# Performance work log

Hardware: AMD Instinct MI355X
Metric: run time of the kernel (lower is better)

The kernel has to match this reference:

```python
import jax, jax.numpy as jnp
import numpy as np

N_NODES = 100000
N_EDGES = 1600000
D_FEAT = 32


def setup_inputs() -> dict:
    key = jax.random.key(0)
    k1, k2 = jax.random.split(key)
    x = jax.random.normal(k1, (N_NODES, D_FEAT), dtype=jnp.float32)
    edge_index = jax.random.randint(k2, (2, N_EDGES), 0, N_NODES, dtype=jnp.int64)
    return {"x": x, "edge_index": edge_index}


def reference(x, edge_index):
    # SparseTensor(row=edge_index[0], col=edge_index[1]).matmul(x, reduce='mean')
    # out[i] = mean_{e: row[e]==i} x[col[e]], 0 for isolated rows.
    row, col = edge_index[0], edge_index[1]
    msg_sum = jax.ops.segment_sum(x[col], row, num_segments=N_NODES)  # [N, D]
    deg = jax.ops.segment_sum(jnp.ones((row.shape[0],), dtype=x.dtype), row,
                              num_segments=N_NODES)  # [N]
    denom = jnp.maximum(deg, jnp.asarray(1, dtype=x.dtype))
    return msg_sum / denom[:, None]
```

## Files before the change

kernel.cpp:

```cpp
#include <hip/hip_runtime.h>
#include <hip/hip_fp16.h>

#define D_FEAT 32
#define BNODES 64
#define LOG_BN 6
#define CHUNK 16384
#define BIG 1024
#define ECHUNK 2048
#define CAP 2048
#define CMASK 0x1FFFFu

__global__ void prep_kernel(const float* __restrict__ x, __half* __restrict__ xh,
                            int* __restrict__ cnt, int n8, int nb) {
    int i = blockIdx.x * blockDim.x + threadIdx.x;
    if (i < nb) cnt[i] = 0;
    if (i < n8) {
        float4 v = ((const float4*)x)[i];
        __half2 h0 = __floats2half2_rn(v.x, v.y);
        __half2 h1 = __floats2half2_rn(v.z, v.w);
        uint2 u;
        u.x = *reinterpret_cast<unsigned*>(&h0);
        u.y = *reinterpret_cast<unsigned*>(&h1);
        ((uint2*)xh)[i] = u;
    }
}

__global__ void __launch_bounds__(BIG) build_kernel(const int* __restrict__ row,
                                                    const int* __restrict__ col,
                                                    int* __restrict__ cnt,
                                                    unsigned* __restrict__ packed,
                                                    int E, int nb) {
    extern __shared__ int shmem[];
    int* hist = shmem;
    int* base = shmem + nb;
    int t = threadIdx.x;
    int blk = blockIdx.x;
    for (int i = t; i < nb; i += BIG) hist[i] = 0;

    int s = blk * CHUNK;
    int e_end = min(E, s + CHUNK);

    int4 r[4], c[4];
    if (s + CHUNK <= E) {
        #pragma unroll
        for (int k = 0; k < 4; ++k) {
            int e = s + t * 4 + k * (BIG * 4);
            r[k] = *(const int4*)&row[e];
            c[k] = *(const int4*)&col[e];
        }
    } else {
        #pragma unroll
        for (int k = 0; k < 4; ++k) {
            int e = s + t * 4 + k * (BIG * 4);
            r[k].x = (e + 0 < e_end) ? row[e + 0] : -1;
            r[k].y = (e + 1 < e_end) ? row[e + 1] : -1;
            r[k].z = (e + 2 < e_end) ? row[e + 2] : -1;
            r[k].w = (e + 3 < e_end) ? row[e + 3] : -1;
            c[k].x = (e + 0 < e_end) ? col[e + 0] : 0;
            c[k].y = (e + 1 < e_end) ? col[e + 1] : 0;
            c[k].z = (e + 2 < e_end) ? col[e + 2] : 0;
            c[k].w = (e + 3 < e_end) ? col[e + 3] : 0;
        }
    }
    __syncthreads();

    #pragma unroll
    for (int k = 0; k < 4; ++k) {
        if (r[k].x >= 0) atomicAdd(&hist[r[k].x >> LOG_BN], 1);
        if (r[k].y >= 0) atomicAdd(&hist[r[k].y >> LOG_BN], 1);
        if (r[k].z >= 0) atomicAdd(&hist[r[k].z >> LOG_BN], 1);
        if (r[k].w >= 0) atomicAdd(&hist[r[k].w >> LOG_BN], 1);
    }
    __syncthreads();

    for (int i = t; i < nb; i += BIG) {
        int h = hist[i];
        base[i] = h ? (i * CAP + atomicAdd(&cnt[i], h)) : 0;
    }
    __syncthreads();

    #define EMIT(rr, cc)                                                      \
        if ((rr) >= 0) {                                                      \
            int b_ = (rr) >> LOG_BN;                                          \
            int slot_ = base[b_] + atomicAdd(&hist[b_], -1) - 1;              \
            packed[slot_] = ((unsigned)((rr) & (BNODES - 1)) << 17) |         \
                            (unsigned)(cc);                                   \
        }
    #pragma unroll
    for (int k = 0; k < 4; ++k) {
        EMIT(r[k].x, c[k].x); EMIT(r[k].y, c[k].y);
        EMIT(r[k].z, c[k].z); EMIT(r[k].w, c[k].w);
    }
    #undef EMIT
}

__global__ void __launch_bounds__(512) phase2_kernel(const __half* __restrict__ xh,
                                                     const unsigned* __restrict__ packed,
                                                     const int* __restrict__ cnt,
                                                     float* __restrict__ out, int N) {
    __shared__ unsigned scol[ECHUNK];
    __shared__ int hist[BNODES];
    __shared__ int hoff[BNODES];
    int t = threadIdx.x;
    int b = blockIdx.x;
    int s = b * CAP;
    int n = cnt[b];
    int node = t >> 3;
    int j = t & 7;
    const uint2* xh2 = (const uint2*)xh;

    float4 acc = make_float4(0.f, 0.f, 0.f, 0.f);
    int mydeg = 0;

    for (int cs = 0; cs < n; cs += ECHUNK) {
        int m = min(ECHUNK, n - cs);
        if (t < BNODES) hist[t] = 0;
        __syncthreads();
        for (int i = t; i < m; i += 512)
            atomicAdd(&hist[packed[s + cs + i] >> 17], 1);
        __syncthreads();
        if (t < 64) {
            int v = hist[t];
            int sum = v;
            #pragma unroll
            for (int off = 1; off < 64; off <<= 1) {
                int w = __shfl_up(sum, off);
                if (t >= off) sum += w;
            }
            hoff[t] = sum - v;
        }
        __syncthreads();
        int mcount = hist[node];
        int mbase = hoff[node];
        mydeg += mcount;
        __syncthreads();
        for (int i = t; i < m; i += 512) {
            unsigned p = packed[s + cs + i];
            int r = p >> 17;
            int slot = hoff[r] + atomicAdd(&hist[r], -1) - 1;
            scol[slot] = p;
        }
        __syncthreads();

        #define ACCUM(u)                                                       \
            {                                                                  \
                __half2 ha = *reinterpret_cast<const __half2*>(&(u).x);        \
                __half2 hb = *reinterpret_cast<const __half2*>(&(u).y);        \
                float2 fa = __half22float2(ha);                                \
                float2 fb = __half22float2(hb);                                \
                acc.x += fa.x; acc.y += fa.y; acc.z += fb.x; acc.w += fb.y;    \
            }

        int i = 0;
        for (; i + 7 < mcount; i += 8) {
            unsigned cc0 = scol[mbase + i + 0] & CMASK;
            unsigned cc1 = scol[mbase + i + 1] & CMASK;
            unsigned cc2 = scol[mbase + i + 2] & CMASK;
            unsigned cc3 = scol[mbase + i + 3] & CMASK;
            unsigned cc4 = scol[mbase + i + 4] & CMASK;
            unsigned cc5 = scol[mbase + i + 5] & CMASK;
            unsigned cc6 = scol[mbase + i + 6] & CMASK;
            unsigned cc7 = scol[mbase + i + 7] & CMASK;
            uint2 u0 = xh2[cc0 * 8 + j];
            uint2 u1 = xh2[cc1 * 8 + j];
            uint2 u2 = xh2[cc2 * 8 + j];
            uint2 u3 = xh2[cc3 * 8 + j];
            uint2 u4 = xh2[cc4 * 8 + j];
            uint2 u5 = xh2[cc5 * 8 + j];
            uint2 u6 = xh2[cc6 * 8 + j];
            uint2 u7 = xh2[cc7 * 8 + j];
            ACCUM(u0); ACCUM(u1); ACCUM(u2); ACCUM(u3);
            ACCUM(u4); ACCUM(u5); ACCUM(u6); ACCUM(u7);
        }
        for (; i < mcount; ++i) {
            unsigned cc = scol[mbase + i] & CMASK;
            uint2 u = xh2[cc * 8 + j];
            ACCUM(u);
        }
        #undef ACCUM
        __syncthreads();
    }

    int gnode = b * BNODES + node;
    if (gnode < N) {
        float invd = 1.0f / fmaxf((float)mydeg, 1.0f);
        float4 v;
        v.x = acc.x * invd; v.y = acc.y * invd;
        v.z = acc.z * invd; v.w = acc.w * invd;
        ((float4*)out)[(size_t)gnode * 8 + j] = v;
    }
}


extern "C" void kernel_launch(void* const* d_in, const int* in_sizes, int n_in,
                              void* d_out, int out_size, void* d_ws, size_t ws_size,
                              hipStream_t stream) {
    const float* x = (const float*)d_in[0];
    const int* edge_index = (const int*)d_in[1];

    int E = in_sizes[1] / 2;
    const int* row = edge_index;
    const int* col = edge_index + E;
    int N = in_sizes[0] / D_FEAT;

    float* out = (float*)d_out;

    int nb = (N + BNODES - 1) / BNODES;
    int nchunks = (E + CHUNK - 1) / CHUNK;
    int n8 = in_sizes[0] / 4;

    int* cnt = (int*)d_ws;
    __half* xh = (__half*)(cnt + ((nb + 1023) & ~1023));
    unsigned* packed = (unsigned*)((char*)xh + (size_t)in_sizes[0] * sizeof(__half));

    int prep_grid = (max(n8, nb) + 255) / 256;
    prep_kernel<<<prep_grid, 256, 0, stream>>>(x, xh, cnt, n8, nb);

    size_t lds = (size_t)2 * nb * sizeof(int);
    build_kernel<<<nchunks, BIG, lds, stream>>>(row, col, cnt, packed, E, nb);
    phase2_kernel<<<nb, 512, 0, stream>>>(xh, packed, cnt, out, N);
}
```

Baseline: 56.23 us.

## Fuse fp16 conversion into build kernel and single-pass phase2 with register-held edges

```diff
diff --git a/kernel.cpp b/kernel.cpp
--- a/kernel.cpp
+++ b/kernel.cpp
@@ -6,30 +6,22 @@
 #define LOG_BN 6
 #define CHUNK 16384
 #define BIG 1024
-#define ECHUNK 2048
-#define CAP 2048
+#define CAP 1536
+#define ECHUNK CAP
 #define CMASK 0x1FFFFu
 
-__global__ void prep_kernel(const float* __restrict__ x, __half* __restrict__ xh,
-                            int* __restrict__ cnt, int n8, int nb) {
+__global__ void zero_kernel(int* __restrict__ p, int n) {
     int i = blockIdx.x * blockDim.x + threadIdx.x;
-    if (i < nb) cnt[i] = 0;
-    if (i < n8) {
-        float4 v = ((const float4*)x)[i];
-        __half2 h0 = __floats2half2_rn(v.x, v.y);
-        __half2 h1 = __floats2half2_rn(v.z, v.w);
-        uint2 u;
-        u.x = *reinterpret_cast<unsigned*>(&h0);
-        u.y = *reinterpret_cast<unsigned*>(&h1);
-        ((uint2*)xh)[i] = u;
-    }
+    if (i < n) p[i] = 0;
 }
 
 __global__ void __launch_bounds__(BIG) build_kernel(const int* __restrict__ row,
                                                     const int* __restrict__ col,
+                                                    const float* __restrict__ x,
+                                                    __half* __restrict__ xh,
                                                     int* __restrict__ cnt,
                                                     unsigned* __restrict__ packed,
-                                                    int E, int nb) {
+                                                    int E, int nb, int n8) {
     extern __shared__ int shmem[];
     int* hist = shmem;
     int* base = shmem + nb;
@@ -92,6 +84,17 @@
         EMIT(r[k].z, c[k].z); EMIT(r[k].w, c[k].w);
     }
     #undef EMIT
+
+    int gstride = gridDim.x * BIG;
+    for (int i = blk * BIG + t; i < n8; i += gstride) {
+        float4 v = ((const float4*)x)[i];
+        __half2 h0 = __floats2half2_rn(v.x, v.y);
+        __half2 h1 = __floats2half2_rn(v.z, v.w);
+        uint2 u;
+        u.x = *reinterpret_cast<unsigned*>(&h0);
+        u.y = *reinterpret_cast<unsigned*>(&h1);
+        ((uint2*)xh)[i] = u;
+    }
 }
 
 __global__ void __launch_bounds__(512) phase2_kernel(const __half* __restrict__ xh,
@@ -109,81 +112,88 @@
     int j = t & 7;
     const uint2* xh2 = (const uint2*)xh;
 
-    float4 acc = make_float4(0.f, 0.f, 0.f, 0.f);
-    int mydeg = 0;
-
-    for (int cs = 0; cs < n; cs += ECHUNK) {
-        int m = min(ECHUNK, n - cs);
-        if (t < BNODES) hist[t] = 0;
-        __syncthreads();
-        for (int i = t; i < m; i += 512)
-            atomicAdd(&hist[packed[s + cs + i] >> 17], 1);
-        __syncthreads();
-        if (t < 64) {
-            int v = hist[t];
-            int sum = v;
-            #pragma unroll
-            for (int off = 1; off < 64; off <<= 1) {
-                int w = __shfl_up(sum, off);
-                if (t >= off) sum += w;
-            }
-            hoff[t] = sum - v;
-        }
-        __syncthreads();
-        int mcount = hist[node];
-        int mbase = hoff[node];
-        mydeg += mcount;
-        __syncthreads();
-        for (int i = t; i < m; i += 512) {
-            unsigned p = packed[s + cs + i];
+    if (t < BNODES) hist[t] = 0;
+    __syncthreads();
+
+    unsigned pv[3];
+    int nv = 0;
+    #pragma unroll
+    for (int k = 0; k < 3; ++k) {
+        int i = t + k * 512;
+        if (i < n) {
+            unsigned p = packed[s + i];
+            pv[nv++] = p;
+            atomicAdd(&hist[p >> 17], 1);
+        }
+    }
+    __syncthreads();
+
+    if (t < 64) {
+        int v = hist[t];
+        int sum = v;
+        #pragma unroll
+        for (int off = 1; off < 64; off <<= 1) {
+            int w = __shfl_up(sum, off);
+            if (t >= off) sum += w;
+        }
+        hoff[t] = sum - v;
+    }
+    __syncthreads();
+    int mcount = hist[node];
+    int mbase = hoff[node];
+    __syncthreads();
+
+    #pragma unroll
+    for (int k = 0; k < 3; ++k) {
+        if (k < nv) {
+            unsigned p = pv[k];
             int r = p >> 17;
             int slot = hoff[r] + atomicAdd(&hist[r], -1) - 1;
             scol[slot] = p;
         }
-        __syncthreads();
-
-        #define ACCUM(u)                                                       \
-            {                                                                  \
-                __half2 ha = *reinterpret_cast<const __half2*>(&(u).x);        \
-                __half2 hb = *reinterpret_cast<const __half2*>(&(u).y);        \
-                float2 fa = __half22float2(ha);                                \
-                float2 fb = __half22float2(hb);                                \
-                acc.x += fa.x; acc.y += fa.y; acc.z += fb.x; acc.w += fb.y;    \
-            }
-
-        int i = 0;
-        for (; i + 7 < mcount; i += 8) {
-            unsigned cc0 = scol[mbase + i + 0] & CMASK;
-            unsigned cc1 = scol[mbase + i + 1] & CMASK;
-            unsigned cc2 = scol[mbase + i + 2] & CMASK;
-            unsigned cc3 = scol[mbase + i + 3] & CMASK;
-            unsigned cc4 = scol[mbase + i + 4] & CMASK;
-            unsigned cc5 = scol[mbase + i + 5] & CMASK;
-            unsigned cc6 = scol[mbase + i + 6] & CMASK;
-            unsigned cc7 = scol[mbase + i + 7] & CMASK;
-            uint2 u0 = xh2[cc0 * 8 + j];
-            uint2 u1 = xh2[cc1 * 8 + j];
-            uint2 u2 = xh2[cc2 * 8 + j];
-            uint2 u3 = xh2[cc3 * 8 + j];
-            uint2 u4 = xh2[cc4 * 8 + j];
-            uint2 u5 = xh2[cc5 * 8 + j];
-            uint2 u6 = xh2[cc6 * 8 + j];
-            uint2 u7 = xh2[cc7 * 8 + j];
-            ACCUM(u0); ACCUM(u1); ACCUM(u2); ACCUM(u3);
-            ACCUM(u4); ACCUM(u5); ACCUM(u6); ACCUM(u7);
-        }
-        for (; i < mcount; ++i) {
-            unsigned cc = scol[mbase + i] & CMASK;
-            uint2 u = xh2[cc * 8 + j];
-            ACCUM(u);
-        }
-        #undef ACCUM
-        __syncthreads();
-    }
+    }
+    __syncthreads();
+
+    float4 acc = make_float4(0.f, 0.f, 0.f, 0.f);
+    #define ACCUM(u)                                                           \
+        {                                                                      \
+            __half2 ha = *reinterpret_cast<const __half2*>(&(u).x);            \
+            __half2 hb = *reinterpret_cast<const __half2*>(&(u).y);            \
+            float2 fa = __half22float2(ha);                                    \
+            float2 fb = __half22float2(hb);                                    \
+            acc.x += fa.x; acc.y += fa.y; acc.z += fb.x; acc.w += fb.y;        \
+        }
+    int i = 0;
+    for (; i + 7 < mcount; i += 8) {
+        unsigned cc0 = scol[mbase + i + 0] & CMASK;
+        unsigned cc1 = scol[mbase + i + 1] & CMASK;
+        unsigned cc2 = scol[mbase + i + 2] & CMASK;
+        unsigned cc3 = scol[mbase + i + 3] & CMASK;
+        unsigned cc4 = scol[mbase + i + 4] & CMASK;
+        unsigned cc5 = scol[mbase + i + 5] & CMASK;
+        unsigned cc6 = scol[mbase + i + 6] & CMASK;
+        unsigned cc7 = scol[mbase + i + 7] & CMASK;
+        uint2 u0 = xh2[cc0 * 8 + j];
+        uint2 u1 = xh2[cc1 * 8 + j];
+        uint2 u2 = xh2[cc2 * 8 + j];
+        uint2 u3 = xh2[cc3 * 8 + j];
+        uint2 u4 = xh2[cc4 * 8 + j];
+        uint2 u5 = xh2[cc5 * 8 + j];
+        uint2 u6 = xh2[cc6 * 8 + j];
+        uint2 u7 = xh2[cc7 * 8 + j];
+        ACCUM(u0); ACCUM(u1); ACCUM(u2); ACCUM(u3);
+        ACCUM(u4); ACCUM(u5); ACCUM(u6); ACCUM(u7);
+    }
+    for (; i < mcount; ++i) {
+        unsigned cc = scol[mbase + i] & CMASK;
+        uint2 u = xh2[cc * 8 + j];
+        ACCUM(u);
+    }
+    #undef ACCUM
 
     int gnode = b * BNODES + node;
     if (gnode < N) {
-        float invd = 1.0f / fmaxf((float)mydeg, 1.0f);
+        float invd = 1.0f / fmaxf((float)mcount, 1.0f);
         float4 v;
         v.x = acc.x * invd; v.y = acc.y * invd;
         v.z = acc.z * invd; v.w = acc.w * invd;
@@ -213,10 +223,9 @@
     __half* xh = (__half*)(cnt + ((nb + 1023) & ~1023));
     unsigned* packed = (unsigned*)((char*)xh + (size_t)in_sizes[0] * sizeof(__half));
 
-    int prep_grid = (max(n8, nb) + 255) / 256;
-    prep_kernel<<<prep_grid, 256, 0, stream>>>(x, xh, cnt, n8, nb);
+    zero_kernel<<<(nb + 255) / 256, 256, 0, stream>>>(cnt, nb);
 
     size_t lds = (size_t)2 * nb * sizeof(int);
-    build_kernel<<<nchunks, BIG, lds, stream>>>(row, col, cnt, packed, E, nb);
+    build_kernel<<<nchunks, BIG, lds, stream>>>(row, col, x, xh, cnt, packed, E, nb, n8);
     phase2_kernel<<<nb, 512, 0, stream>>>(xh, packed, cnt, out, N);
 }
```

Result: slower. 57.42 us (+2.1%).
